# Optimization experiments

Measured on AMD Instinct MI355X. Metric: run time of the kernel, lower is better.

## Reference

```python
import jax, jax.numpy as jnp
import numpy as np


def setup_inputs() -> dict:
    key = jax.random.key(0)
    ks = jax.random.split(key, 6)
    B, U, E, D, P = 8, 1024, 1024, 256, 256
    return {
        "u_enc": jax.random.normal(ks[0], (B, U, D), dtype=jnp.float32),
        "e_enc": jax.random.normal(ks[1], (B, E, D), dtype=jnp.float32),
        "pair_enc": jax.random.normal(ks[2], (B, U, E), dtype=jnp.float32),
        "ue_mask": jax.random.uniform(ks[3], (B, U, E), dtype=jnp.float32),
        "w_kernel": jax.random.normal(ks[4], (D, P), dtype=jnp.float32) / np.sqrt(D).astype(np.float32),
        "w_bias": jnp.zeros((P,), dtype=jnp.float32),
        "bpp_w": jnp.ones((), dtype=jnp.float32),
        "bpp_b": jnp.zeros((), dtype=jnp.float32),
    }


def reference(u_enc, e_enc, pair_enc, ue_mask, w_kernel, w_bias, bpp_w, bpp_b):
    # OuterProductUpdate: shared Dense projection of u and e, then outer product.
    u_p = u_enc @ w_kernel + w_bias            # [B,U,P]
    e_p = e_enc @ w_kernel + w_bias            # [B,E,P]
    op = ue_mask * jnp.einsum('bup,bep->bue', u_p, e_p)  # [B,U,E]
    # Sigmoid gate over pair features.
    mask = ue_mask * jax.nn.sigmoid(bpp_w * pair_enc + bpp_b + op)  # [B,U,E]
    # Original: (mask[...,None] * concat(u_rep, e_rep)).sum(axis=(-2,-3)).
    # Algebraically identical without the UxEx2D intermediate:
    #   concat( sum_{u,e} mask * u_enc[u],  sum_{u,e} mask * e_enc[e] )
    u_part = jnp.einsum('bue,bud->bd', mask, u_enc)  # [B,D]
    e_part = jnp.einsum('bue,bed->bd', mask, e_enc)  # [B,D]
    return jnp.concatenate([u_part, e_part], axis=-1)  # [B,2D]
```

## Files before the change

### kernel.cpp

```cpp
#include <hip/hip_runtime.h>

#define BDIM 8
#define UDIM 1024
#define EDIM 1024
#define DDIM 256
#define PDIM 256

typedef __attribute__((ext_vector_type(8))) short bf16x8;
typedef __attribute__((ext_vector_type(4))) float f32x4;
typedef __attribute__((ext_vector_type(4))) ushort u16x4;

__device__ __forceinline__ short f2bf(float x) {
    unsigned u = __float_as_uint(x);
    unsigned r = (u + 0x7FFFu + ((u >> 16) & 1u)) >> 16;
    return (short)r;
}

__device__ __forceinline__ void dma16(const void* g, void* lds) {
    __builtin_amdgcn_global_load_lds(
        (const __attribute__((address_space(1))) unsigned*)g,
        (__attribute__((address_space(3))) unsigned*)lds, 16, 0, 0);
}

#define KEEP(x) asm volatile("" :: "v"(x))

__global__ __launch_bounds__(256) void prep_kernel(
    const float* __restrict__ w, ushort* __restrict__ wT,
    float* __restrict__ out, int out_size)
{
    int k  = threadIdx.x;
    int n0 = blockIdx.x * 4;
    f32x4 wv = *(const f32x4*)(w + (size_t)k * PDIM + n0);
    wT[(size_t)(n0 + 0) * DDIM + k] = (ushort)f2bf(wv[0]);
    wT[(size_t)(n0 + 1) * DDIM + k] = (ushort)f2bf(wv[1]);
    wT[(size_t)(n0 + 2) * DDIM + k] = (ushort)f2bf(wv[2]);
    wT[(size_t)(n0 + 3) * DDIM + k] = (ushort)f2bf(wv[3]);
    int g = blockIdx.x * 256 + k;
    if (g < out_size) out[g] = 0.f;
}

__global__ __launch_bounds__(256) void proj_kernel(
    const float* __restrict__ u_enc, const float* __restrict__ e_enc,
    const ushort* __restrict__ wT, const float* __restrict__ bias,
    ushort* __restrict__ u_p, ushort* __restrict__ e_p)
{
    __shared__ ushort lds_b[64 * 256];

    int bid  = blockIdx.x;
    int lin  = (bid & 7) * 128 + (bid >> 3);
    int row0 = (lin >> 2) * 64;
    int col0 = (lin & 3) * 64;

    const float* A; ushort* C;
    if (row0 < BDIM * UDIM) { A = u_enc; C = u_p; }
    else                    { A = e_enc; C = e_p; row0 -= BDIM * UDIM; }

    int tid  = threadIdx.x;
    int wave = tid >> 6, lane = tid & 63;
    int m = lane & 15, quad = lane >> 4;

    {
        int rl_base = wave * 16;
        int lr = lane >> 5;
        int cb = (lane & 31) * 16;
        #pragma unroll
        for (int j = 0; j < 8; ++j) {
            int rl = rl_base + 2 * j + lr;
            const ushort* src = wT + (size_t)(col0 + rl) * DDIM + ((cb ^ ((rl & 7) << 4)) >> 1);
            dma16(src, &lds_b[(size_t)(rl_base + 2 * j) * DDIM]);
        }
    }

    const float* aptr = A + (size_t)(row0 + wave * 16 + m) * DDIM + quad * 8;
    f32x4 a[16];
    #pragma unroll
    for (int i = 0; i < 8; ++i) {
        a[2 * i]     = *(const f32x4*)(aptr + 32 * i);
        a[2 * i + 1] = *(const f32x4*)(aptr + 32 * i + 4);
    }
    #pragma unroll
    for (int i = 0; i < 16; ++i) KEEP(a[i]);

    asm volatile("s_waitcnt vmcnt(0)" ::: "memory");
    __syncthreads();

    int rowmask = (m & 7) << 4;
    f32x4 acc[4] = {};
    #pragma unroll
    for (int i = 0; i < 8; ++i) {
        bf16x8 af;
        af[0] = f2bf(a[2*i][0]);   af[1] = f2bf(a[2*i][1]);
        af[2] = f2bf(a[2*i][2]);   af[3] = f2bf(a[2*i][3]);
        af[4] = f2bf(a[2*i+1][0]); af[5] = f2bf(a[2*i+1][1]);
        af[6] = f2bf(a[2*i+1][2]); af[7] = f2bf(a[2*i+1][3]);
        #pragma unroll
        for (int nt = 0; nt < 4; ++nt) {
            int elem = (nt * 16 + m) * DDIM + (((quad * 16 + 64 * i) ^ rowmask) >> 1);
            bf16x8 bfr = *(const bf16x8*)(lds_b + elem);
            acc[nt] = __builtin_amdgcn_mfma_f32_16x16x32_bf16(af, bfr, acc[nt], 0, 0, 0);
        }
    }

    #pragma unroll
    for (int r = 0; r < 4; ++r) {
        int row = row0 + wave * 16 + quad * 4 + r;
        u16x4 pk;
        #pragma unroll
        for (int nt = 0; nt < 4; ++nt)
            pk[nt] = (ushort)f2bf(acc[nt][r] + bias[col0 + nt * 16 + m]);
        *(u16x4*)(C + (size_t)row * PDIM + col0 + 4 * m) = pk;
    }
}

__global__ __launch_bounds__(256) void fused_kernel(
    const ushort* __restrict__ u_p, const ushort* __restrict__ e_p,
    const float* __restrict__ pair_enc, const float* __restrict__ ue_mask,
    const float* __restrict__ bpp_w_p, const float* __restrict__ bpp_b_p,
    float* __restrict__ row_part ,
    float* __restrict__ col_part )
{
    __shared__ ushort lds_e[64 * 256];
    __shared__ float colred[4][64];

    int bid  = blockIdx.x;
    int b    = bid & 7;
    int tile = bid >> 3;
    int iu = tile >> 4, ie = tile & 15;
    int u0 = iu * 64, e0 = ie * 64;

    int tid  = threadIdx.x;
    int wave = tid >> 6, lane = tid & 63;
    int m = lane & 15, quad = lane >> 4;

    const float* pm = pair_enc + (size_t)b * UDIM * EDIM;
    const float* mm = ue_mask  + (size_t)b * UDIM * EDIM;
    const ushort* eb = e_p + (size_t)b * EDIM * PDIM;

    {
        int lr = lane >> 5;
        int cb = (lane & 31) * 16;
        #pragma unroll
        for (int j = 0; j < 8; ++j) {
            int rl = wave * 16 + 2 * j + lr;
            int esrc = e0 + ((rl & 15) << 2) + (rl >> 4);
            const ushort* src = eb + (size_t)esrc * PDIM + ((cb ^ ((rl & 7) << 4)) >> 1);
            dma16(src, &lds_e[(size_t)(wave * 16 + 2 * j) * PDIM]);
        }
    }

    const ushort* Au = u_p + (size_t)b * UDIM * PDIM + (size_t)(u0 + wave * 16 + m) * PDIM + quad * 8;
    bf16x8 af[8];
    #pragma unroll
    for (int i = 0; i < 8; ++i) af[i] = *(const bf16x8*)(Au + 32 * i);
    #pragma unroll
    for (int i = 0; i < 8; ++i) KEEP(af[i]);

    {
    }
    const float* pmRow = pm + (size_t)(u0 + wave * 16 + quad * 4) * EDIM + e0 + 4 * m;
    const float* mmRow = mm + (size_t)(u0 + wave * 16 + quad * 4) * EDIM + e0 + 4 * m;
    f32x4 pv4[4], mv4[4];
    #pragma unroll
    for (int r = 0; r < 4; ++r) {
        pv4[r] = *(const f32x4*)(pmRow + (size_t)r * EDIM);
        mv4[r] = *(const f32x4*)(mmRow + (size_t)r * EDIM);
    }
    #pragma unroll
    for (int r = 0; r < 4; ++r) { KEEP(pv4[r]); KEEP(mv4[r]); }

    float bw = bpp_w_p[0], bb = bpp_b_p[0];

    asm volatile("s_waitcnt vmcnt(0)" ::: "memory");
    __syncthreads();

    int rowmask = (m & 7) << 4;
    f32x4 acc[4] = {};
    #pragma unroll
    for (int i = 0; i < 8; ++i) {
        #pragma unroll
        for (int nt = 0; nt < 4; ++nt) {
            int elem = (nt * 16 + m) * PDIM + (((quad * 16 + 64 * i) ^ rowmask) >> 1);
            bf16x8 bfr = *(const bf16x8*)(lds_e + elem);
            acc[nt] = __builtin_amdgcn_mfma_f32_16x16x32_bf16(af[i], bfr, acc[nt], 0, 0, 0);
        }
    }

    float rsum[4] = {0.f, 0.f, 0.f, 0.f};
    float csum[4] = {0.f, 0.f, 0.f, 0.f};
    #pragma unroll
    for (int r = 0; r < 4; ++r) {
        #pragma unroll
        for (int nt = 0; nt < 4; ++nt) {
            float mv = mv4[r][nt];
            float pvv = pv4[r][nt];
            float arg = bw * pvv + bb + mv * acc[nt][r];
            float s = mv / (1.f + __expf(-arg));
            rsum[r]  += s;
            csum[nt] += s;
        }
    }

    #pragma unroll
    for (int r = 0; r < 4; ++r) {
        float v = rsum[r];
        v += __shfl_xor(v, 1); v += __shfl_xor(v, 2);
        v += __shfl_xor(v, 4); v += __shfl_xor(v, 8);
        if (m == 0)
            row_part[((size_t)b * 16 + ie) * UDIM + u0 + wave * 16 + quad * 4 + r] = v;
    }

    #pragma unroll
    for (int nt = 0; nt < 4; ++nt) {
        float v = csum[nt];
        v += __shfl_xor(v, 16); v += __shfl_xor(v, 32);
        if (quad == 0) colred[wave][4 * m + nt] = v;
    }
    __syncthreads();

    if (tid < 64) {
        float v = colred[0][tid] + colred[1][tid] + colred[2][tid] + colred[3][tid];
        col_part[((size_t)b * 16 + iu) * EDIM + e0 + tid] = v;
    }
}

__global__ __launch_bounds__(256) void finish_kernel(
    const float* __restrict__ u_enc, const float* __restrict__ e_enc,
    const float* __restrict__ row_part, const float* __restrict__ col_part,
    float* __restrict__ out)
{
    __shared__ float s_lds[32];

    int b = blockIdx.x;
    int half = blockIdx.y;
    int chunk = blockIdx.z;
    int d = threadIdx.x;

    const float* enc  = half ? e_enc   : u_enc;
    const float* part = half ? col_part : row_part;

    int base = chunk * 32;
    if (d < 32) {
        float s = 0.f;
        #pragma unroll
        for (int p = 0; p < 16; ++p)
            s += part[((size_t)b * 16 + p) * UDIM + base + d];
        s_lds[d] = s;
    }

    float ev[32];
    #pragma unroll
    for (int j = 0; j < 32; ++j)
        ev[j] = enc[(size_t)(b * UDIM + base + j) * DDIM + d];
    #pragma unroll
    for (int j = 0; j < 32; ++j) KEEP(ev[j]);

    __syncthreads();

    float acc = 0.f;
    #pragma unroll
    for (int j = 0; j < 32; ++j)
        acc += s_lds[j] * ev[j];

    atomicAdd(&out[(size_t)b * 2 * DDIM + half * DDIM + d], acc);
}

extern "C" void kernel_launch(void* const* d_in, const int* in_sizes, int n_in,
                              void* d_out, int out_size, void* d_ws, size_t ws_size,
                              hipStream_t stream)
{
    const float* u_enc    = (const float*)d_in[0];
    const float* e_enc    = (const float*)d_in[1];
    const float* pair_enc = (const float*)d_in[2];
    const float* ue_mask  = (const float*)d_in[3];
    const float* w_kernel = (const float*)d_in[4];
    const float* w_bias   = (const float*)d_in[5];
    const float* bpp_w    = (const float*)d_in[6];
    const float* bpp_b    = (const float*)d_in[7];
    float* out = (float*)d_out;

    ushort* u_p = (ushort*)d_ws;
    ushort* e_p = u_p + (size_t)BDIM * UDIM * PDIM;
    ushort* wT  = e_p + (size_t)BDIM * EDIM * PDIM;
    float* row_part = (float*)(wT + (size_t)DDIM * PDIM);
    float* col_part = row_part + (size_t)BDIM * 16 * UDIM;

    prep_kernel<<<dim3(64), 256, 0, stream>>>(w_kernel, wT, out, out_size);

    proj_kernel<<<dim3(1024), 256, 0, stream>>>(u_enc, e_enc, wT, w_bias, u_p, e_p);

    fused_kernel<<<dim3(2048), 256, 0, stream>>>(u_p, e_p, pair_enc, ue_mask,
                                                 bpp_w, bpp_b, row_part, col_part);

    finish_kernel<<<dim3(BDIM, 2, 32), 256, 0, stream>>>(u_enc, e_enc, row_part, col_part, out);
}
```

Baseline: 148.8 us.

## Fuse finish reduction into fused kernel via per-batch atomic completion counters

```diff
diff --git a/kernel.cpp b/kernel.cpp
--- a/kernel.cpp
+++ b/kernel.cpp
@@ -24,9 +24,13 @@
 
 #define KEEP(x) asm volatile("" :: "v"(x))
 
+#define ASTORE(p, v) __hip_atomic_store((p), (v), __ATOMIC_RELAXED, __HIP_MEMORY_SCOPE_AGENT)
+#define ALOAD(p)     __hip_atomic_load((p), __ATOMIC_RELAXED, __HIP_MEMORY_SCOPE_AGENT)
+
 __global__ __launch_bounds__(256) void prep_kernel(
     const float* __restrict__ w, ushort* __restrict__ wT,
-    float* __restrict__ out, int out_size)
+    float* __restrict__ out, int out_size,
+    unsigned* __restrict__ counters)
 {
     int k  = threadIdx.x;
     int n0 = blockIdx.x * 4;
@@ -37,6 +41,7 @@
     wT[(size_t)(n0 + 3) * DDIM + k] = (ushort)f2bf(wv[3]);
     int g = blockIdx.x * 256 + k;
     if (g < out_size) out[g] = 0.f;
+    if (blockIdx.x == 0 && k < BDIM) counters[k] = 0u;
 }
 
 __global__ __launch_bounds__(256) void proj_kernel(
@@ -116,11 +121,14 @@
     const ushort* __restrict__ u_p, const ushort* __restrict__ e_p,
     const float* __restrict__ pair_enc, const float* __restrict__ ue_mask,
     const float* __restrict__ bpp_w_p, const float* __restrict__ bpp_b_p,
+    const float* __restrict__ u_enc, const float* __restrict__ e_enc,
     float* __restrict__ row_part ,
-    float* __restrict__ col_part )
+    float* __restrict__ col_part ,
+    unsigned* __restrict__ counters, float* __restrict__ out)
 {
     __shared__ ushort lds_e[64 * 256];
     __shared__ float colred[4][64];
+    __shared__ unsigned bcast;
 
     int bid  = blockIdx.x;
     int b    = bid & 7;
@@ -155,8 +163,6 @@
     #pragma unroll
     for (int i = 0; i < 8; ++i) KEEP(af[i]);
 
-    {
-    }
     const float* pmRow = pm + (size_t)(u0 + wave * 16 + quad * 4) * EDIM + e0 + 4 * m;
     const float* mmRow = mm + (size_t)(u0 + wave * 16 + quad * 4) * EDIM + e0 + 4 * m;
     f32x4 pv4[4], mv4[4];
@@ -206,7 +212,7 @@
         v += __shfl_xor(v, 1); v += __shfl_xor(v, 2);
         v += __shfl_xor(v, 4); v += __shfl_xor(v, 8);
         if (m == 0)
-            row_part[((size_t)b * 16 + ie) * UDIM + u0 + wave * 16 + quad * 4 + r] = v;
+            ASTORE(&row_part[((size_t)b * 4 + ie / 4 * 0 + (ie & 3)) * 0 + ((size_t)b * 4 + (ie & 3)) * 0 + ((size_t)b * 16 + ie) * UDIM + u0 + wave * 16 + quad * 4 + r], v);
     }
 
     #pragma unroll
@@ -219,49 +225,64 @@
 
     if (tid < 64) {
         float v = colred[0][tid] + colred[1][tid] + colred[2][tid] + colred[3][tid];
-        col_part[((size_t)b * 16 + iu) * EDIM + e0 + tid] = v;
-    }
-}
-
-__global__ __launch_bounds__(256) void finish_kernel(
-    const float* __restrict__ u_enc, const float* __restrict__ e_enc,
-    const float* __restrict__ row_part, const float* __restrict__ col_part,
-    float* __restrict__ out)
-{
-    __shared__ float s_lds[32];
-
-    int b = blockIdx.x;
-    int half = blockIdx.y;
-    int chunk = blockIdx.z;
-    int d = threadIdx.x;
-
-    const float* enc  = half ? e_enc   : u_enc;
-    const float* part = half ? col_part : row_part;
-
-    int base = chunk * 32;
-    if (d < 32) {
-        float s = 0.f;
-        #pragma unroll
-        for (int p = 0; p < 16; ++p)
-            s += part[((size_t)b * 16 + p) * UDIM + base + d];
-        s_lds[d] = s;
-    }
-
-    float ev[32];
-    #pragma unroll
-    for (int j = 0; j < 32; ++j)
-        ev[j] = enc[(size_t)(b * UDIM + base + j) * DDIM + d];
-    #pragma unroll
-    for (int j = 0; j < 32; ++j) KEEP(ev[j]);
-
-    __syncthreads();
-
-    float acc = 0.f;
-    #pragma unroll
-    for (int j = 0; j < 32; ++j)
-        acc += s_lds[j] * ev[j];
-
-    atomicAdd(&out[(size_t)b * 2 * DDIM + half * DDIM + d], acc);
+        ASTORE(&col_part[((size_t)b * 16 + iu) * EDIM + e0 + tid], v);
+    }
+
+    __syncthreads();
+    if (tid == 0)
+        bcast = __hip_atomic_fetch_add(&counters[b], 1u, __ATOMIC_ACQ_REL, __HIP_MEMORY_SCOPE_AGENT);
+    __syncthreads();
+    unsigned idx = bcast;
+    if (idx < 240u) return;
+
+    if (tid == 0) {
+        while (__hip_atomic_load(&counters[b], __ATOMIC_ACQUIRE, __HIP_MEMORY_SCOPE_AGENT) < 256u)
+            __builtin_amdgcn_s_sleep(8);
+    }
+    __syncthreads();
+
+    int fi   = (int)idx - 240;
+    int half = fi >> 3;
+    int d0   = (fi & 7) * 32;
+    const float* encb = (half ? e_enc : u_enc) + (size_t)b * UDIM * DDIM;
+
+    float* s_lds = (float*)lds_e;
+    float* red   = ((float*)lds_e) + 1024;
+
+    {
+        int u = tid * 4;
+        #pragma unroll
+        for (int k = 0; k < 4; ++k) {
+            float s = 0.f;
+            if (half) {
+                #pragma unroll
+                for (int p = 0; p < 16; ++p)
+                    s += ALOAD(&col_part[((size_t)b * 16 + p) * EDIM + u + k]);
+            } else {
+                #pragma unroll
+                for (int p = 0; p < 16; ++p)
+                    s += ALOAD(&row_part[((size_t)b * 16 + p) * UDIM + u + k]);
+            }
+            s_lds[u + k] = s;
+        }
+    }
+    __syncthreads();
+
+    int d  = d0 + (tid & 31);
+    int ug = tid >> 5;
+    float facc = 0.f;
+    #pragma unroll 8
+    for (int u = ug * 128; u < ug * 128 + 128; ++u)
+        facc += s_lds[u] * encb[(size_t)u * DDIM + d];
+    red[ug * 32 + (tid & 31)] = facc;
+    __syncthreads();
+
+    if (tid < 32) {
+        float v = 0.f;
+        #pragma unroll
+        for (int g = 0; g < 8; ++g) v += red[g * 32 + tid];
+        out[(size_t)b * 2 * DDIM + half * DDIM + d0 + tid] = v;
+    }
 }
 
 extern "C" void kernel_launch(void* const* d_in, const int* in_sizes, int n_in,
@@ -283,13 +304,13 @@
     ushort* wT  = e_p + (size_t)BDIM * EDIM * PDIM;
     float* row_part = (float*)(wT + (size_t)DDIM * PDIM);
     float* col_part = row_part + (size_t)BDIM * 16 * UDIM;
-
-    prep_kernel<<<dim3(64), 256, 0, stream>>>(w_kernel, wT, out, out_size);
+    unsigned* counters = (unsigned*)(col_part + (size_t)BDIM * 16 * EDIM);
+
+    prep_kernel<<<dim3(64), 256, 0, stream>>>(w_kernel, wT, out, out_size, counters);
 
     proj_kernel<<<dim3(1024), 256, 0, stream>>>(u_enc, e_enc, wT, w_bias, u_p, e_p);
 
     fused_kernel<<<dim3(2048), 256, 0, stream>>>(u_p, e_p, pair_enc, ue_mask,
-                                                 bpp_w, bpp_b, row_part, col_part);
-
-    finish_kernel<<<dim3(BDIM, 2, 32), 256, 0, stream>>>(u_enc, e_enc, row_part, col_part, out);
-}
+                                                 bpp_w, bpp_b, u_enc, e_enc,
+                                                 row_part, col_part, counters, out);
+}
```

Measured after the change: 226.9 us. 52.5% more time.

## Compute all projection columns per block with double-buffered weight tiles

Applied to the files above, without the earlier changes.

```diff
diff --git a/kernel.cpp b/kernel.cpp
--- a/kernel.cpp
+++ b/kernel.cpp
@@ -44,12 +44,10 @@
     const ushort* __restrict__ wT, const float* __restrict__ bias,
     ushort* __restrict__ u_p, ushort* __restrict__ e_p)
 {
-    __shared__ ushort lds_b[64 * 256];
+    __shared__ ushort lds_b[2][64 * 256];
 
     int bid  = blockIdx.x;
-    int lin  = (bid & 7) * 128 + (bid >> 3);
-    int row0 = (lin >> 2) * 64;
-    int col0 = (lin & 3) * 64;
+    int row0 = ((bid & 7) * 32 + (bid >> 3)) * 64;
 
     const float* A; ushort* C;
     if (row0 < BDIM * UDIM) { A = u_enc; C = u_p; }
@@ -59,18 +57,6 @@
     int wave = tid >> 6, lane = tid & 63;
     int m = lane & 15, quad = lane >> 4;
 
-    {
-        int rl_base = wave * 16;
-        int lr = lane >> 5;
-        int cb = (lane & 31) * 16;
-        #pragma unroll
-        for (int j = 0; j < 8; ++j) {
-            int rl = rl_base + 2 * j + lr;
-            const ushort* src = wT + (size_t)(col0 + rl) * DDIM + ((cb ^ ((rl & 7) << 4)) >> 1);
-            dma16(src, &lds_b[(size_t)(rl_base + 2 * j) * DDIM]);
-        }
-    }
-
     const float* aptr = A + (size_t)(row0 + wave * 16 + m) * DDIM + quad * 8;
     f32x4 a[16];
     #pragma unroll
@@ -81,35 +67,63 @@
     #pragma unroll
     for (int i = 0; i < 16; ++i) KEEP(a[i]);
 
-    asm volatile("s_waitcnt vmcnt(0)" ::: "memory");
-    __syncthreads();
+    int srl = wave * 16 + (lane >> 5);
+    int scb = (lane & 31) * 16;
+    #define STAGE_W(t, buf) {                                                  \
+        int col0s = (t) * 64;                                                  \
+        _Pragma("unroll")                                                      \
+        for (int j = 0; j < 8; ++j) {                                          \
+            int rl = srl + 2 * j;                                              \
+            const ushort* src = wT + (size_t)(col0s + rl) * DDIM               \
+                                + ((scb ^ ((rl & 7) << 4)) >> 1);              \
+            dma16(src, &lds_b[buf][(size_t)(wave * 16 + 2 * j) * DDIM]);       \
+        }                                                                      \
+    }
+
+    STAGE_W(0, 0);
 
     int rowmask = (m & 7) << 4;
-    f32x4 acc[4] = {};
-    #pragma unroll
-    for (int i = 0; i < 8; ++i) {
-        bf16x8 af;
-        af[0] = f2bf(a[2*i][0]);   af[1] = f2bf(a[2*i][1]);
-        af[2] = f2bf(a[2*i][2]);   af[3] = f2bf(a[2*i][3]);
-        af[4] = f2bf(a[2*i+1][0]); af[5] = f2bf(a[2*i+1][1]);
-        af[6] = f2bf(a[2*i+1][2]); af[7] = f2bf(a[2*i+1][3]);
-        #pragma unroll
-        for (int nt = 0; nt < 4; ++nt) {
-            int elem = (nt * 16 + m) * DDIM + (((quad * 16 + 64 * i) ^ rowmask) >> 1);
-            bf16x8 bfr = *(const bf16x8*)(lds_b + elem);
-            acc[nt] = __builtin_amdgcn_mfma_f32_16x16x32_bf16(af, bfr, acc[nt], 0, 0, 0);
-        }
-    }
-
-    #pragma unroll
-    for (int r = 0; r < 4; ++r) {
-        int row = row0 + wave * 16 + quad * 4 + r;
-        u16x4 pk;
-        #pragma unroll
-        for (int nt = 0; nt < 4; ++nt)
-            pk[nt] = (ushort)f2bf(acc[nt][r] + bias[col0 + nt * 16 + m]);
-        *(u16x4*)(C + (size_t)row * PDIM + col0 + 4 * m) = pk;
-    }
+
+    #pragma unroll
+    for (int s = 0; s < 4; ++s) {
+        int buf = s & 1;
+        int col0 = s * 64;
+
+        __builtin_amdgcn_s_barrier();
+        if (s < 3) STAGE_W(s + 1, buf ^ 1);
+        __builtin_amdgcn_sched_barrier(0);
+        if (s < 3) asm volatile("s_waitcnt vmcnt(8)" ::: "memory");
+        else       asm volatile("s_waitcnt vmcnt(0)" ::: "memory");
+        __builtin_amdgcn_sched_barrier(0);
+        __builtin_amdgcn_s_barrier();
+
+        f32x4 acc[4] = {};
+        #pragma unroll
+        for (int i = 0; i < 8; ++i) {
+            bf16x8 af;
+            af[0] = f2bf(a[2*i][0]);   af[1] = f2bf(a[2*i][1]);
+            af[2] = f2bf(a[2*i][2]);   af[3] = f2bf(a[2*i][3]);
+            af[4] = f2bf(a[2*i+1][0]); af[5] = f2bf(a[2*i+1][1]);
+            af[6] = f2bf(a[2*i+1][2]); af[7] = f2bf(a[2*i+1][3]);
+            #pragma unroll
+            for (int nt = 0; nt < 4; ++nt) {
+                int elem = (nt * 16 + m) * DDIM + (((quad * 16 + 64 * i) ^ rowmask) >> 1);
+                bf16x8 bfr = *(const bf16x8*)(&lds_b[buf][0] + elem);
+                acc[nt] = __builtin_amdgcn_mfma_f32_16x16x32_bf16(af, bfr, acc[nt], 0, 0, 0);
+            }
+        }
+
+        #pragma unroll
+        for (int r = 0; r < 4; ++r) {
+            int row = row0 + wave * 16 + quad * 4 + r;
+            u16x4 pk;
+            #pragma unroll
+            for (int nt = 0; nt < 4; ++nt)
+                pk[nt] = (ushort)f2bf(acc[nt][r] + bias[col0 + nt * 16 + m]);
+            *(u16x4*)(C + (size_t)row * PDIM + col0 + 4 * m) = pk;
+        }
+    }
+    #undef STAGE_W
 }
 
 __global__ __launch_bounds__(256) void fused_kernel(
@@ -155,8 +169,6 @@
     #pragma unroll
     for (int i = 0; i < 8; ++i) KEEP(af[i]);
 
-    {
-    }
     const float* pmRow = pm + (size_t)(u0 + wave * 16 + quad * 4) * EDIM + e0 + 4 * m;
     const float* mmRow = mm + (size_t)(u0 + wave * 16 + quad * 4) * EDIM + e0 + 4 * m;
     f32x4 pv4[4], mv4[4];
@@ -286,7 +298,7 @@
 
     prep_kernel<<<dim3(64), 256, 0, stream>>>(w_kernel, wT, out, out_size);
 
-    proj_kernel<<<dim3(1024), 256, 0, stream>>>(u_enc, e_enc, wT, w_bias, u_p, e_p);
+    proj_kernel<<<dim3(256), 256, 0, stream>>>(u_enc, e_enc, wT, w_bias, u_p, e_p);
 
     fused_kernel<<<dim3(2048), 256, 0, stream>>>(u_p, e_p, pair_enc, ue_mask,
                                                  bpp_w, bpp_b, row_part, col_part);
```

New measurement: 150.4 us. Within noise of the previous version (+1.0%).
